# Optimization experiments

Hardware: AMD Instinct MI355X
Metric: run time of the kernel (lower is better)

Reference implementation:

```python
import jax, jax.numpy as jnp
import numpy as np


def _pairwise_sqdist(x, y):
    # x: [B, Nx, D] (gts), y: [B, Ny, D] (preds)
    # P[b,i,j] = ||x[b,i]||^2 + ||y[b,j]||^2 - 2 <x[b,i], y[b,j]>
    rx = jnp.sum(x * x, axis=-1)  # [B, Nx]
    ry = jnp.sum(y * y, axis=-1)  # [B, Ny]
    zz = jnp.einsum('bid,bjd->bij', x, y)  # [B, Nx, Ny]
    return rx[:, :, None] + ry[:, None, :] - 2.0 * zz


def setup_inputs() -> dict:
    key = jax.random.key(0)
    k1, k2 = jax.random.split(key)
    B, N, D = 8, 8192, 3
    preds = jax.random.normal(k1, (B, N, D), dtype=jnp.float32)
    gts = jax.random.normal(k2, (B, N, D), dtype=jnp.float32)
    return {"preds": preds, "gts": gts}


def reference(preds, gts):
    # Original: P = batch_pairwise_dist(gts, preds) -> [B, N_gts, N_preds]
    P = _pairwise_sqdist(gts, preds)
    loss_1 = jnp.sum(jnp.min(P, axis=1))  # min over gts points, per pred point
    loss_2 = jnp.sum(jnp.min(P, axis=2))  # min over pred points, per gt point
    return loss_1 + loss_2
```

## Files before the change

### kernel.cpp

```cpp
#include <hip/hip_runtime.h>

#define NPTS   8192
#define NBATCH 8
#define BLKT   512
#define CHUNK  2048
#define NCHUNK (NPTS / CHUNK)
#define CPT    (CHUNK / BLKT)

typedef __attribute__((ext_vector_type(8)))  short bf16x8;
typedef __attribute__((ext_vector_type(16))) float f32x16;

__device__ __forceinline__ void bsplit(float v, unsigned int& h, unsigned int& l) {
    unsigned int u = __float_as_uint(v);
    h = u >> 16;
    float rem = v - __uint_as_float(u & 0xFFFF0000u);
    l = __float_as_uint(rem) >> 16;
}


__global__ __launch_bounds__(BLKT, 2) void chamfer_r11(
    const float* __restrict__ preds,
    const float* __restrict__ gts,
    float* __restrict__ out)
{
    __shared__ uint4 lds4[4608];
    unsigned short* lds = (unsigned short*)lds4;
    float* fbuf = (float*)lds4;

    const int tid  = threadIdx.x;
    const int wave = tid >> 6;
    const int lane = tid & 63;
    const int n    = lane & 31;
    const int h    = lane >> 5;
    const int rg   = wave & 3;
    const int cf   = wave >> 2;

    const int rchunk = blockIdx.x;
    const int batch  = blockIdx.y;
    const int dir    = blockIdx.z;

    const float* rows = ((dir == 0) ? gts   : preds) + (size_t)batch * NPTS * 3;
    const float* cols = ((dir == 0) ? preds : gts)   + (size_t)batch * NPTS * 3;
    const int ibase = rchunk * 256;
    const unsigned int ONE = 0x3F80u;
    const int B_HI = 16384, A_LO = 32768, A_HI = 34816;

    float R[3 * CPT];
    #pragma unroll
    for (int j = 0; j < CPT; ++j) {
        int c = j * BLKT + tid;
        R[j * 3 + 0] = cols[c * 3 + 0];
        R[j * 3 + 1] = cols[c * 3 + 1];
        R[j * 3 + 2] = cols[c * 3 + 2];
    }

    if (tid < 256) {
        int gi = ibase + tid;
        float x = rows[gi * 3 + 0], y = rows[gi * 3 + 1], z = rows[gi * 3 + 2];
        float g2 = x * x + y * y + z * z;
        unsigned int xh, xl, yh, yl, zh, zl, gh, gl;
        bsplit(x, xh, xl); bsplit(y, yh, yl); bsplit(z, zh, zl); bsplit(g2, gh, gl);
        lds4[4096 + tid] = make_uint4(xh | (yh << 16), zh | (gh << 16),
                                      ONE | (xh << 16), yh | (zh << 16));
        lds4[4352 + tid] = make_uint4(gh | (ONE << 16), xl | (yl << 16),
                                      zl | (gl << 16), 0u);
    }
    __syncthreads();

    bf16x8 afr[2];
    #pragma unroll
    for (int t = 0; t < 2; ++t) {
        int row = rg * 64 + t * 32 + n;
        afr[t] = *(const bf16x8*)&lds[(h ? A_HI : A_LO) + row * 8];
    }
    f32x16 rmin[2];
    #pragma unroll
    for (int t = 0; t < 2; ++t)
        #pragma unroll
        for (int e = 0; e < 16; ++e) rmin[t][e] = 3.4e38f;

    const f32x16 zeroC = (f32x16)(0.f);
    const unsigned short* bp = &lds[(h ? B_HI : 0) + (cf * 1024 + n) * 8];

    for (int ch = 0; ch < NCHUNK; ++ch) {
        #pragma unroll
        for (int j = 0; j < CPT; ++j) {
            int c = j * BLKT + tid;
            float x = R[j * 3 + 0], y = R[j * 3 + 1], z = R[j * 3 + 2];
            float p2 = x * x + y * y + z * z;
            unsigned int cxh, cxl, cyh, cyl, czh, czl, ph, pl;
            bsplit(-2.f * x, cxh, cxl); bsplit(-2.f * y, cyh, cyl);
            bsplit(-2.f * z, czh, czl); bsplit(p2, ph, pl);
            lds4[c]        = make_uint4(cxh | (cyh << 16), czh | (ONE << 16),
                                        ph | (cxl << 16), cyl | (czl << 16));
            lds4[2048 + c] = make_uint4(pl << 16, cxh | (cyh << 16),
                                        czh | (ONE << 16), ph);
        }
        __syncthreads();

        if (ch < NCHUNK - 1) {
            #pragma unroll
            for (int j = 0; j < CPT; ++j) {
                int c = (ch + 1) * CHUNK + j * BLKT + tid;
                R[j * 3 + 0] = cols[c * 3 + 0];
                R[j * 3 + 1] = cols[c * 3 + 1];
                R[j * 3 + 2] = cols[c * 3 + 2];
            }
        }

        #pragma unroll 2
        for (int jt2 = 0; jt2 < 16; ++jt2) {
            bf16x8 b0 = *(const bf16x8*)(bp + jt2 * 512);
            bf16x8 b1 = *(const bf16x8*)(bp + jt2 * 512 + 256);
            #pragma unroll
            for (int t = 0; t < 2; ++t) {
                f32x16 ca = __builtin_amdgcn_mfma_f32_32x32x16_bf16(afr[t], b0, zeroC, 0, 0, 0);
                f32x16 cb = __builtin_amdgcn_mfma_f32_32x32x16_bf16(afr[t], b1, zeroC, 0, 0, 0);
                #pragma unroll
                for (int e = 0; e < 16; ++e)
                    rmin[t][e] = fminf(fminf(ca[e], cb[e]), rmin[t][e]);
            }
        }
        __syncthreads();
    }

    #pragma unroll
    for (int t = 0; t < 2; ++t) {
        #pragma unroll
        for (int e = 0; e < 16; ++e) {
            float v = rmin[t][e];
            v = fminf(v, __shfl_xor(v, 1, 64));
            v = fminf(v, __shfl_xor(v, 2, 64));
            v = fminf(v, __shfl_xor(v, 4, 64));
            v = fminf(v, __shfl_xor(v, 8, 64));
            v = fminf(v, __shfl_xor(v, 16, 64));
            if (n == 0) {
                int row = rg * 64 + t * 32 + (e & 3) + 8 * (e >> 2) + 4 * h;
                fbuf[cf * 256 + row] = v;
            }
        }
    }
    __syncthreads();

    float s = 0.f;
    if (tid < 256) s = fminf(fbuf[tid], fbuf[256 + tid]);
    #pragma unroll
    for (int off = 32; off > 0; off >>= 1)
        s += __shfl_down(s, off, 64);
    if (lane == 0) fbuf[512 + wave] = s;
    __syncthreads();
    if (tid == 0) {
        float tot = 0.f;
        #pragma unroll
        for (int w = 0; w < 8; ++w) tot += fbuf[512 + w];
        atomicAdd(out, tot);
    }
}

extern "C" void kernel_launch(void* const* d_in, const int* in_sizes, int n_in,
                              void* d_out, int out_size, void* d_ws, size_t ws_size,
                              hipStream_t stream) {
    const float* preds = (const float*)d_in[0];
    const float* gts   = (const float*)d_in[1];
    float* out = (float*)d_out;

    dim3 grid(NPTS / 256, NBATCH, 2);
    chamfer_r11<<<grid, dim3(BLKT), 0, stream>>>(preds, gts, out);
}
```

Before: 94.85 us.

## Shrink row tile to 128 and column chunk to 1024, raise occupancy, drop register prefetch

Each block now covers 128 row points instead of 256, and the column chunk staged in LDS shrinks to 1024 points, so the LDS footprint halves. Launch bounds go from 2 to 6 blocks per CU, and the grid doubles, to hide latency through occupancy. The register prefetch of the next column chunk is removed; columns are loaded straight from global memory inside the chunk loop. The trade-off is more redundant column reprocessing per row (twice as many blocks each recompute bf16 splits of all columns) and more syncs per block.

```diff
diff --git a/kernel.cpp b/kernel.cpp
--- a/kernel.cpp
+++ b/kernel.cpp
@@ -3,7 +3,8 @@
 #define NPTS   8192
 #define NBATCH 8
 #define BLKT   512
-#define CHUNK  2048
+#define ROWS   128
+#define CHUNK  1024
 #define NCHUNK (NPTS / CHUNK)
 #define CPT    (CHUNK / BLKT)
 
@@ -18,12 +19,12 @@
 }
 
 
-__global__ __launch_bounds__(BLKT, 2) void chamfer_r11(
+__global__ __launch_bounds__(BLKT, 6) void chamfer_r12(
     const float* __restrict__ preds,
     const float* __restrict__ gts,
     float* __restrict__ out)
 {
-    __shared__ uint4 lds4[4608];
+    __shared__ uint4 lds4[2304];
     unsigned short* lds = (unsigned short*)lds4;
     float* fbuf = (float*)lds4;
 
@@ -32,8 +33,8 @@
     const int lane = tid & 63;
     const int n    = lane & 31;
     const int h    = lane >> 5;
-    const int rg   = wave & 3;
-    const int cf   = wave >> 2;
+    const int rg   = wave & 1;
+    const int cf   = wave >> 1;
 
     const int rchunk = blockIdx.x;
     const int batch  = blockIdx.y;
@@ -41,28 +42,19 @@
 
     const float* rows = ((dir == 0) ? gts   : preds) + (size_t)batch * NPTS * 3;
     const float* cols = ((dir == 0) ? preds : gts)   + (size_t)batch * NPTS * 3;
-    const int ibase = rchunk * 256;
+    const int ibase = rchunk * ROWS;
     const unsigned int ONE = 0x3F80u;
-    const int B_HI = 16384, A_LO = 32768, A_HI = 34816;
+    const int B_HI = 8192, A_LO = 16384, A_HI = 17408;
 
-    float R[3 * CPT];
-    #pragma unroll
-    for (int j = 0; j < CPT; ++j) {
-        int c = j * BLKT + tid;
-        R[j * 3 + 0] = cols[c * 3 + 0];
-        R[j * 3 + 1] = cols[c * 3 + 1];
-        R[j * 3 + 2] = cols[c * 3 + 2];
-    }
-
-    if (tid < 256) {
+    if (tid < ROWS) {
         int gi = ibase + tid;
         float x = rows[gi * 3 + 0], y = rows[gi * 3 + 1], z = rows[gi * 3 + 2];
         float g2 = x * x + y * y + z * z;
         unsigned int xh, xl, yh, yl, zh, zl, gh, gl;
         bsplit(x, xh, xl); bsplit(y, yh, yl); bsplit(z, zh, zl); bsplit(g2, gh, gl);
-        lds4[4096 + tid] = make_uint4(xh | (yh << 16), zh | (gh << 16),
+        lds4[2048 + tid] = make_uint4(xh | (yh << 16), zh | (gh << 16),
                                       ONE | (xh << 16), yh | (zh << 16));
-        lds4[4352 + tid] = make_uint4(gh | (ONE << 16), xl | (yl << 16),
+        lds4[2176 + tid] = make_uint4(gh | (ONE << 16), xl | (yl << 16),
                                       zl | (gl << 16), 0u);
     }
     __syncthreads();
@@ -80,36 +72,27 @@
         for (int e = 0; e < 16; ++e) rmin[t][e] = 3.4e38f;
 
     const f32x16 zeroC = (f32x16)(0.f);
-    const unsigned short* bp = &lds[(h ? B_HI : 0) + (cf * 1024 + n) * 8];
+    const unsigned short* bp = &lds[(h ? B_HI : 0) + (cf * 256 + n) * 8];
 
     for (int ch = 0; ch < NCHUNK; ++ch) {
         #pragma unroll
         for (int j = 0; j < CPT; ++j) {
-            int c = j * BLKT + tid;
-            float x = R[j * 3 + 0], y = R[j * 3 + 1], z = R[j * 3 + 2];
+            int c  = j * BLKT + tid;
+            int gc = ch * CHUNK + c;
+            float x = cols[gc * 3 + 0], y = cols[gc * 3 + 1], z = cols[gc * 3 + 2];
             float p2 = x * x + y * y + z * z;
             unsigned int cxh, cxl, cyh, cyl, czh, czl, ph, pl;
             bsplit(-2.f * x, cxh, cxl); bsplit(-2.f * y, cyh, cyl);
             bsplit(-2.f * z, czh, czl); bsplit(p2, ph, pl);
             lds4[c]        = make_uint4(cxh | (cyh << 16), czh | (ONE << 16),
                                         ph | (cxl << 16), cyl | (czl << 16));
-            lds4[2048 + c] = make_uint4(pl << 16, cxh | (cyh << 16),
+            lds4[1024 + c] = make_uint4(pl << 16, cxh | (cyh << 16),
                                         czh | (ONE << 16), ph);
         }
         __syncthreads();
 
-        if (ch < NCHUNK - 1) {
-            #pragma unroll
-            for (int j = 0; j < CPT; ++j) {
-                int c = (ch + 1) * CHUNK + j * BLKT + tid;
-                R[j * 3 + 0] = cols[c * 3 + 0];
-                R[j * 3 + 1] = cols[c * 3 + 1];
-                R[j * 3 + 2] = cols[c * 3 + 2];
-            }
-        }
-
-        #pragma unroll 2
-        for (int jt2 = 0; jt2 < 16; ++jt2) {
+        #pragma unroll
+        for (int jt2 = 0; jt2 < 4; ++jt2) {
             bf16x8 b0 = *(const bf16x8*)(bp + jt2 * 512);
             bf16x8 b1 = *(const bf16x8*)(bp + jt2 * 512 + 256);
             #pragma unroll
@@ -136,25 +119,24 @@
             v = fminf(v, __shfl_xor(v, 16, 64));
             if (n == 0) {
                 int row = rg * 64 + t * 32 + (e & 3) + 8 * (e >> 2) + 4 * h;
-                fbuf[cf * 256 + row] = v;
+                fbuf[cf * ROWS + row] = v;
             }
         }
     }
     __syncthreads();
 
     float s = 0.f;
-    if (tid < 256) s = fminf(fbuf[tid], fbuf[256 + tid]);
+    if (tid < ROWS) {
+        s = fminf(fminf(fbuf[tid], fbuf[ROWS + tid]),
+                  fminf(fbuf[2 * ROWS + tid], fbuf[3 * ROWS + tid]));
+    }
     #pragma unroll
     for (int off = 32; off > 0; off >>= 1)
         s += __shfl_down(s, off, 64);
-    if (lane == 0) fbuf[512 + wave] = s;
+    if (lane == 0 && wave < 2) fbuf[512 + wave] = s;
     __syncthreads();
-    if (tid == 0) {
-        float tot = 0.f;
-        #pragma unroll
-        for (int w = 0; w < 8; ++w) tot += fbuf[512 + w];
-        atomicAdd(out, tot);
-    }
+    if (tid == 0)
+        atomicAdd(out, fbuf[512] + fbuf[513]);
 }
 
 extern "C" void kernel_launch(void* const* d_in, const int* in_sizes, int n_in,
@@ -164,6 +146,6 @@
     const float* gts   = (const float*)d_in[1];
     float* out = (float*)d_out;
 
-    dim3 grid(NPTS / 256, NBATCH, 2);
-    chamfer_r11<<<grid, dim3(BLKT), 0, stream>>>(preds, gts, out);
+    dim3 grid(NPTS / ROWS, NBATCH, 2);
+    chamfer_r12<<<grid, dim3(BLKT), 0, stream>>>(preds, gts, out);
 }
```

New measurement: 139.4 us. 47.0% more time.
